# Performance work log

Hardware: AMD Instinct MI355X
Metric: run time of the kernel (lower is better)

## Reference

```python
import jax, jax.numpy as jnp
import numpy as np

D_MODEL = 1024
NUM_HEADS = 16
HEAD_DIM = D_MODEL // NUM_HEADS


def setup_inputs() -> dict:
    key = jax.random.key(0)
    ks = jax.random.split(key, 5)
    B, S = 4, 2048
    x = jax.random.normal(ks[0], (B, S, D_MODEL), dtype=jnp.float32)
    scale = 1.0 / np.sqrt(D_MODEL)
    qkv_w = jax.random.normal(ks[1], (3 * D_MODEL, D_MODEL), dtype=jnp.float32) * scale
    qkv_b = jnp.zeros((3 * D_MODEL,), dtype=jnp.float32)
    out_w = jax.random.normal(ks[2], (D_MODEL, D_MODEL), dtype=jnp.float32) * scale
    out_b = jnp.zeros((D_MODEL,), dtype=jnp.float32)
    return {"x": x, "qkv_w": qkv_w, "qkv_b": qkv_b, "out_w": out_w, "out_b": out_b}


def reference(x, qkv_w, qkv_b, out_w, out_b):
    B, S, _ = x.shape
    # qkv projection (torch Linear: x @ W.T + b)
    qkv = x @ qkv_w.T + qkv_b  # [B, S, 3*D]
    q, k, v = jnp.split(qkv, 3, axis=-1)
    # [B, H, S, hd]
    q = q.reshape(B, S, NUM_HEADS, HEAD_DIM).transpose(0, 2, 1, 3)
    k = k.reshape(B, S, NUM_HEADS, HEAD_DIM).transpose(0, 2, 1, 3)
    v = v.reshape(B, S, NUM_HEADS, HEAD_DIM).transpose(0, 2, 1, 3)
    scores = jnp.einsum('bhqd,bhkd->bhqk', q, k) / np.sqrt(HEAD_DIM).astype(np.float32)
    attn = jax.nn.softmax(scores, axis=-1)
    context = jnp.einsum('bhqk,bhkd->bhqd', attn, v)  # [B, H, S, hd]
    context = context.transpose(0, 2, 1, 3).reshape(B, S, D_MODEL)
    return context @ out_w.T + out_b
```

## Files before the change

### kernel.cpp

```cpp
#include <hip/hip_runtime.h>
#include <hip/hip_bf16.h>
#include <math.h>

#define D_MODEL 1024
#define NHEADS  16
#define HDIM    64
#define BATCH   4
#define SLEN    2048
#define MROWS   (BATCH * SLEN)
#define QKV_N   (3 * D_MODEL)

typedef __attribute__((ext_vector_type(8))) short bhalf8;
typedef __attribute__((ext_vector_type(4))) float f32x4;

#if __has_builtin(__builtin_amdgcn_exp2f)
#define EXP2(x) __builtin_amdgcn_exp2f(x)
#else
#define EXP2(x) exp2f(x)
#endif

#define MFMA16(a, b, c) __builtin_amdgcn_mfma_f32_16x16x32_bf16((a), (b), (c), 0, 0, 0)

static __device__ __forceinline__ unsigned short f2bf(float f) {
    unsigned int u = __builtin_bit_cast(unsigned int, f);
    unsigned int r = (u + 0x7FFFu + ((u >> 16) & 1u)) >> 16;
    return (unsigned short)r;
}

static __device__ __forceinline__ unsigned int pack_hi16(float lo, float hi) {
    return __builtin_amdgcn_perm(__builtin_bit_cast(unsigned int, hi),
                                 __builtin_bit_cast(unsigned int, lo),
                                 0x07060302u);
}

static __device__ __forceinline__ void load_lds16(const void* g, void* l) {
    __builtin_amdgcn_global_load_lds(
        (const __attribute__((address_space(1))) void*)g,
        (__attribute__((address_space(3))) void*)l, 16, 0, 0);
}

#define FENCE() __asm__ volatile("" ::: "memory")
#define BARRIER() do { FENCE();                                   \
        __builtin_amdgcn_sched_barrier(0);                        \
        __builtin_amdgcn_s_barrier();                             \
        __builtin_amdgcn_sched_barrier(0); FENCE(); } while (0)
#define WAIT_VM(N)   __asm__ volatile("s_waitcnt vmcnt(" #N ")" ::: "memory")
#define WAIT_LGKM0() __asm__ volatile("s_waitcnt lgkmcnt(0)" ::: "memory")

__global__ __launch_bounds__(256) void cast_f32_bf16(
    const float* __restrict__ in, unsigned short* __restrict__ out, int n)
{
    int i = (blockIdx.x * 256 + threadIdx.x) * 4;
    if (i < n) {
        float4 v = *(const float4*)(in + i);
        ushort4 o;
        o.x = f2bf(v.x); o.y = f2bf(v.y); o.z = f2bf(v.z); o.w = f2bf(v.w);
        *(ushort4*)(out + i) = o;
    }
}

template<bool BF16OUT>
__global__ __launch_bounds__(256) void gemm_mfma_bt(
    const unsigned short* __restrict__ A,
    const unsigned short* __restrict__ W,
    const float* __restrict__ bias,
    void* __restrict__ outv,
    int M, int N, int K, int qcols, float qscale)
{
    __shared__ __align__(16) unsigned short As[128 * 32];
    __shared__ __align__(16) unsigned short Bs[128 * 32];

    const int tid  = threadIdx.x;
    const int bm   = blockIdx.y * 128;
    const int bn   = blockIdx.x * 128;
    const int wave = tid >> 6;
    const int lane = tid & 63;
    const int m16  = lane & 15;
    const int quad = lane >> 4;
    const int wm   = (wave & 1) * 64;
    const int wn   = (wave >> 1) * 64;

    const int r0 = tid >> 2;
    const int s0 = tid & 3;
    const int g0 = (s0 - (r0 >> 1)) & 3;
    const int g1 = (s0 - ((r0 + 64) >> 1)) & 3;

    const size_t arow0 = (size_t)(bm + r0) * K + g0 * 8;
    const size_t arow1 = (size_t)(bm + r0 + 64) * K + g1 * 8;
    const size_t brow0 = (size_t)(bn + r0) * K + g0 * 8;
    const size_t brow1 = (size_t)(bn + r0 + 64) * K + g1 * 8;

    f32x4 acc[4][4];
    f32x4 zero = {0.f, 0.f, 0.f, 0.f};
#pragma unroll
    for (int i = 0; i < 4; ++i)
#pragma unroll
        for (int j = 0; j < 4; ++j) acc[i][j] = zero;

    for (int kt = 0; kt < K; kt += 32) {
        __syncthreads();
        load_lds16(A + arow0 + kt, As + tid * 8);
        load_lds16(A + arow1 + kt, As + 2048 + tid * 8);
        load_lds16(W + brow0 + kt, Bs + tid * 8);
        load_lds16(W + brow1 + kt, Bs + 2048 + tid * 8);
        __asm__ volatile("s_waitcnt vmcnt(0)" ::: "memory");
        __syncthreads();

        bhalf8 af[4], bf[4];
#pragma unroll
        for (int i = 0; i < 4; ++i) {
            int ra = wm + i * 16 + m16;
            int sa = (quad + (ra >> 1)) & 3;
            af[i] = *(const bhalf8*)&As[ra * 32 + sa * 8];
        }
#pragma unroll
        for (int j = 0; j < 4; ++j) {
            int rb = wn + j * 16 + m16;
            int sb = (quad + (rb >> 1)) & 3;
            bf[j] = *(const bhalf8*)&Bs[rb * 32 + sb * 8];
        }
#pragma unroll
        for (int i = 0; i < 4; ++i)
#pragma unroll
            for (int j = 0; j < 4; ++j)
                acc[i][j] = __builtin_amdgcn_mfma_f32_16x16x32_bf16(
                    af[i], bf[j], acc[i][j], 0, 0, 0);
    }

    float bj[4], scj[4];
#pragma unroll
    for (int j = 0; j < 4; ++j) {
        int col = bn + wn + j * 16 + m16;
        bj[j]  = bias[col];
        scj[j] = (col < qcols) ? qscale : 1.0f;
    }

#pragma unroll
    for (int i = 0; i < 4; ++i) {
#pragma unroll
        for (int r = 0; r < 4; ++r) {
            size_t row = (size_t)(bm + wm + i * 16 + quad * 4 + r);
            if (BF16OUT) {
                unsigned short* dst = (unsigned short*)outv + row * N + bn + wn;
#pragma unroll
                for (int j = 0; j < 4; ++j)
                    dst[j * 16 + m16] = f2bf((acc[i][j][r] + bj[j]) * scj[j]);
            } else {
                float* dst = (float*)outv + row * N + bn + wn;
#pragma unroll
                for (int j = 0; j < 4; ++j)
                    dst[j * 16 + m16] = (acc[i][j][r] + bj[j]) * scj[j];
            }
        }
    }
}

__global__ __launch_bounds__(256, 4) void attn_mfma_kernel(
    const unsigned short* __restrict__ qkv, unsigned short* __restrict__ ctx)
{
    const int orig = blockIdx.x + (blockIdx.y << 4) + (blockIdx.z << 8);
    const int flat = ((orig & 7) << 7) | (orig >> 3);
    const int qt = flat & 15;
    const int h  = (flat >> 4) & 15;
    const int b  = flat >> 8;

    const int tid  = threadIdx.x;
    const int wave = tid >> 6;
    const int lane = tid & 63;
    const int m16  = lane & 15;
    const int quad = lane >> 4;

    __shared__ __align__(16) unsigned short K_lds[64 * 64];
    __shared__ __align__(16) unsigned short Vt_lds[64 * 72];
    __shared__ __align__(16) unsigned short QP_lds[4 * 32 * 72];

    const int srow  = tid >> 3;
    const int sslot = tid & 7;
    const int gk    = (sslot - srow) & 7;

    const int u    = tid & 31;
    const int k0   = (u & 15) | ((u & 16) << 1);
    const int idx0 = (u & 15) * 4 + ((u >> 4) << 1);
    const int vd0  = (tid >> 5) * 8;

    const unsigned short* kPtr =
        qkv + ((size_t)b * SLEN) * QKV_N + D_MODEL + h * HDIM
            + (size_t)srow * QKV_N + gk * 8;
    const unsigned short* vPtr0 =
        qkv + ((size_t)b * SLEN) * QKV_N + 2 * D_MODEL + h * HDIM
            + (size_t)k0 * QKV_N + vd0;
    const unsigned short* vPtr1 = vPtr0 + (size_t)16 * QKV_N;

    uint4 va_A, vb_A, va_B, vb_B;

#define ISSUE_K(T) do {                                                      \
        const unsigned short* kb_ = kPtr + (size_t)(T) * 64 * QKV_N;         \
        load_lds16(kb_,                        K_lds + tid * 8);             \
        load_lds16(kb_ + (size_t)32 * QKV_N,   K_lds + 2048 + tid * 8);      \
    } while (0)

#define ISSUE_V(T, VA, VB) do {                                              \
        VA = *(const uint4*)(vPtr0 + (size_t)(T) * 64 * QKV_N);              \
        VB = *(const uint4*)(vPtr1 + (size_t)(T) * 64 * QKV_N);              \
    } while (0)

#define WRITE_V(VA, VB) do {                                                                         \
        *(unsigned int*)&Vt_lds[(vd0 + 0) * 72 + idx0] = __builtin_amdgcn_perm(VB.x, VA.x, 0x05040100u); \
        *(unsigned int*)&Vt_lds[(vd0 + 1) * 72 + idx0] = __builtin_amdgcn_perm(VB.x, VA.x, 0x07060302u); \
        *(unsigned int*)&Vt_lds[(vd0 + 2) * 72 + idx0] = __builtin_amdgcn_perm(VB.y, VA.y, 0x05040100u); \
        *(unsigned int*)&Vt_lds[(vd0 + 3) * 72 + idx0] = __builtin_amdgcn_perm(VB.y, VA.y, 0x07060302u); \
        *(unsigned int*)&Vt_lds[(vd0 + 4) * 72 + idx0] = __builtin_amdgcn_perm(VB.z, VA.z, 0x05040100u); \
        *(unsigned int*)&Vt_lds[(vd0 + 5) * 72 + idx0] = __builtin_amdgcn_perm(VB.z, VA.z, 0x07060302u); \
        *(unsigned int*)&Vt_lds[(vd0 + 6) * 72 + idx0] = __builtin_amdgcn_perm(VB.w, VA.w, 0x05040100u); \
        *(unsigned int*)&Vt_lds[(vd0 + 7) * 72 + idx0] = __builtin_amdgcn_perm(VB.w, VA.w, 0x07060302u); \
    } while (0)

    {
        const unsigned short* qbase =
            qkv + (size_t)(b * SLEN + qt * 128) * QKV_N + h * HDIM;
#pragma unroll
        for (int c = 0; c < 4; ++c) {
            int r = c * 32 + srow;
            int g = (sslot - r) & 7;
            load_lds16(qbase + (size_t)r * QKV_N + g * 8,
                       QP_lds + c * 2048 + tid * 8);
        }
    }
    ISSUE_K(0);
    ISSUE_V(0, va_A, vb_A);
    WAIT_VM(2);
    BARRIER();

    bhalf8 qf[2][2];
#pragma unroll
    for (int qi = 0; qi < 2; ++qi) {
        int rq = wave * 32 + qi * 16 + m16;
#pragma unroll
        for (int ks = 0; ks < 2; ++ks) {
            int slot = (ks * 4 + quad + rq) & 7;
            qf[qi][ks] = *(const bhalf8*)&QP_lds[rq * 64 + slot * 8];
        }
    }

    WAIT_VM(0);
    WRITE_V(va_A, vb_A);
    ISSUE_V(1, va_B, vb_B);
    WAIT_LGKM0();
    BARRIER();

    f32x4 zero = {0.f, 0.f, 0.f, 0.f};
    f32x4 oacc[2][4], oacc_l[2];
#pragma unroll
    for (int qi = 0; qi < 2; ++qi) {
        oacc_l[qi] = zero;
#pragma unroll
        for (int dt = 0; dt < 4; ++dt) oacc[qi][dt] = zero;
    }

    bhalf8 ones;
#pragma unroll
    for (int i = 0; i < 8; ++i) ones[i] = (short)0x3F80;

    unsigned short* P = &QP_lds[wave * (32 * 72)];
    f32x4 sacc[2][4];

#define QKT_PHASE() do {                                                     \
        _Pragma("unroll")                                                    \
        for (int qi = 0; qi < 2; ++qi)                                       \
            _Pragma("unroll")                                                \
            for (int nt = 0; nt < 4; ++nt) sacc[qi][nt] = zero;              \
        __builtin_amdgcn_s_setprio(1);                                       \
        _Pragma("unroll")                                                    \
        for (int ks = 0; ks < 2; ++ks) {                                     \
            _Pragma("unroll")                                                \
            for (int nt = 0; nt < 4; ++nt) {                                 \
                int rk = nt * 16 + m16;                                      \
                int slot = (ks * 4 + quad + rk) & 7;                         \
                bhalf8 kf = *(const bhalf8*)&K_lds[rk * 64 + slot * 8];      \
                sacc[0][nt] = MFMA16(qf[0][ks], kf, sacc[0][nt]);            \
                sacc[1][nt] = MFMA16(qf[1][ks], kf, sacc[1][nt]);            \
            }                                                                \
        }                                                                    \
        __builtin_amdgcn_s_setprio(0);                                       \
    } while (0)

#define SOFTMAX_PHASE() do {                                                 \
        _Pragma("unroll")                                                    \
        for (int qi = 0; qi < 2; ++qi) {                                     \
            _Pragma("unroll")                                                \
            for (int r = 0; r < 4; ++r) {                                    \
                float p0 = EXP2(sacc[qi][0][r]);                             \
                float p1 = EXP2(sacc[qi][1][r]);                             \
                float p2 = EXP2(sacc[qi][2][r]);                             \
                float p3 = EXP2(sacc[qi][3][r]);                             \
                uint2 w;                                                     \
                w.x = pack_hi16(p0, p1);                                     \
                w.y = pack_hi16(p2, p3);                                     \
                *(uint2*)&P[(qi * 16 + quad * 4 + r) * 72 + m16 * 4] = w;    \
            }                                                                \
        }                                                                    \
        WAIT_LGKM0();                                                        \
        __builtin_amdgcn_sched_barrier(0);                                   \
    } while (0)

#define PV_PHASE() do {                                                      \
        __builtin_amdgcn_s_setprio(1);                                       \
        _Pragma("unroll")                                                    \
        for (int ks = 0; ks < 2; ++ks) {                                     \
            bhalf8 pf0 = *(const bhalf8*)&P[(m16)      * 72 + ks * 32 + quad * 8]; \
            bhalf8 pf1 = *(const bhalf8*)&P[(16 + m16) * 72 + ks * 32 + quad * 8]; \
            oacc_l[0] = MFMA16(pf0, ones, oacc_l[0]);                        \
            oacc_l[1] = MFMA16(pf1, ones, oacc_l[1]);                        \
            _Pragma("unroll")                                                \
            for (int dt = 0; dt < 4; ++dt) {                                 \
                bhalf8 vf = *(const bhalf8*)&Vt_lds[(dt * 16 + m16) * 72 + ks * 32 + quad * 8]; \
                oacc[0][dt] = MFMA16(pf0, vf, oacc[0][dt]);                  \
                oacc[1][dt] = MFMA16(pf1, vf, oacc[1][dt]);                  \
            }                                                                \
        }                                                                    \
        __builtin_amdgcn_s_setprio(0);                                       \
    } while (0)

#define TILE_FULL(T, VAW, VBW, VAL, VBL) do {                                \
        QKT_PHASE();                                                         \
        BARRIER();                     \
        ISSUE_K((T) + 1);                                                    \
        SOFTMAX_PHASE();                                                     \
        PV_PHASE();                                                          \
        BARRIER();                     \
        WAIT_VM(2);                    \
        WRITE_V(VAW, VBW);                                                   \
        ISSUE_V((T) + 2, VAL, VBL);                                          \
        WAIT_VM(2);                    \
        WAIT_LGKM0();                                                        \
        BARRIER();                     \
    } while (0)

    for (int t2 = 0; t2 < 30; t2 += 2) {
        TILE_FULL(t2,     va_B, vb_B, va_A, vb_A);
        TILE_FULL(t2 + 1, va_A, vb_A, va_B, vb_B);
    }

    QKT_PHASE();
    BARRIER();
    ISSUE_K(31);
    SOFTMAX_PHASE();
    PV_PHASE();
    BARRIER();
    WAIT_VM(2);
    WRITE_V(va_B, vb_B);
    WAIT_VM(0);
    WAIT_LGKM0();
    BARRIER();

    QKT_PHASE();
    SOFTMAX_PHASE();
    PV_PHASE();

#undef TILE_FULL
#undef PV_PHASE
#undef SOFTMAX_PHASE
#undef QKT_PHASE
#undef WRITE_V
#undef ISSUE_V
#undef ISSUE_K

#pragma unroll
    for (int qi = 0; qi < 2; ++qi) {
#pragma unroll
        for (int r = 0; r < 4; ++r) {
            float inv = 1.0f / oacc_l[qi][r];
            int row = b * SLEN + qt * 128 + wave * 32 + qi * 16 + quad * 4 + r;
            unsigned short* dst = ctx + (size_t)row * D_MODEL + h * HDIM;
#pragma unroll
            for (int dt = 0; dt < 4; ++dt)
                dst[dt * 16 + m16] = f2bf(oacc[qi][dt][r] * inv);
        }
    }
}

extern "C" void kernel_launch(void* const* d_in, const int* in_sizes, int n_in,
                              void* d_out, int out_size, void* d_ws, size_t ws_size,
                              hipStream_t stream)
{
    const float* x     = (const float*)d_in[0];
    const float* qkv_w = (const float*)d_in[1];
    const float* qkv_b = (const float*)d_in[2];
    const float* out_w = (const float*)d_in[3];
    const float* out_b = (const float*)d_in[4];
    float* out = (float*)d_out;

    unsigned short* xbf  = (unsigned short*)d_ws;
    unsigned short* wqkv = xbf  + (size_t)MROWS * D_MODEL;
    unsigned short* wout = wqkv + (size_t)QKV_N * D_MODEL;
    unsigned short* qkv  = wout + (size_t)D_MODEL * D_MODEL;
    unsigned short* ctx  = qkv  + (size_t)MROWS * QKV_N;

    {
        int n;
        n = MROWS * D_MODEL;
        cast_f32_bf16<<<n / 1024, 256, 0, stream>>>(x, xbf, n);
        n = QKV_N * D_MODEL;
        cast_f32_bf16<<<n / 1024, 256, 0, stream>>>(qkv_w, wqkv, n);
        n = D_MODEL * D_MODEL;
        cast_f32_bf16<<<n / 1024, 256, 0, stream>>>(out_w, wout, n);
    }

    const float QSCALE = 0.125f * 1.44269504088896f;

    {
        dim3 grid(QKV_N / 128, MROWS / 128);
        gemm_mfma_bt<true><<<grid, 256, 0, stream>>>(xbf, wqkv, qkv_b, qkv,
                                                     MROWS, QKV_N, D_MODEL,
                                                     D_MODEL, QSCALE);
    }

    {
        dim3 grid(SLEN / 128, NHEADS, BATCH);
        attn_mfma_kernel<<<grid, 256, 0, stream>>>(qkv, ctx);
    }

    {
        dim3 grid(D_MODEL / 128, MROWS / 128);
        gemm_mfma_bt<false><<<grid, 256, 0, stream>>>(ctx, wout, out_b, out,
                                                      MROWS, D_MODEL, D_MODEL,
                                                      0, 1.0f);
    }
}
```

Baseline: 280.7 us.

## Double-buffer K/V tiles in attention and merge cast kernels into one launch

The attention kernel now keeps two LDS buffers for K and transposed V. This lets the next K tile be prefetched before the QK^T phase and removes two of the three barriers per tile, overlapping loads with compute. Separately, the three fp32-to-bf16 cast launches are merged into one kernel to cut launch overhead. The extra LDS (about 17 KB more per block) may lower occupancy below the declared 4 blocks per CU.

```diff
diff --git a/kernel.cpp b/kernel.cpp
--- a/kernel.cpp
+++ b/kernel.cpp
@@ -47,16 +47,25 @@
 #define WAIT_VM(N)   __asm__ volatile("s_waitcnt vmcnt(" #N ")" ::: "memory")
 #define WAIT_LGKM0() __asm__ volatile("s_waitcnt lgkmcnt(0)" ::: "memory")
 
-__global__ __launch_bounds__(256) void cast_f32_bf16(
-    const float* __restrict__ in, unsigned short* __restrict__ out, int n)
+__global__ __launch_bounds__(256) void cast3_f32_bf16(
+    const float* __restrict__ a, unsigned short* __restrict__ oa, int na,
+    const float* __restrict__ b, unsigned short* __restrict__ ob, int nb,
+    const float* __restrict__ c, unsigned short* __restrict__ oc, int nc)
 {
     int i = (blockIdx.x * 256 + threadIdx.x) * 4;
-    if (i < n) {
-        float4 v = *(const float4*)(in + i);
-        ushort4 o;
-        o.x = f2bf(v.x); o.y = f2bf(v.y); o.z = f2bf(v.z); o.w = f2bf(v.w);
-        *(ushort4*)(out + i) = o;
-    }
+    const float* src;
+    unsigned short* dst;
+    if (i < na)           { src = a + i;            dst = oa + i; }
+    else if (i < na + nb) { src = b + (i - na);     dst = ob + (i - na); }
+    else {
+        int j = i - na - nb;
+        if (j >= nc) return;
+        src = c + j; dst = oc + j;
+    }
+    float4 v = *(const float4*)src;
+    ushort4 o;
+    o.x = f2bf(v.x); o.y = f2bf(v.y); o.z = f2bf(v.z); o.w = f2bf(v.w);
+    *(ushort4*)dst = o;
 }
 
 template<bool BF16OUT>
@@ -170,8 +179,8 @@
     const int m16  = lane & 15;
     const int quad = lane >> 4;
 
-    __shared__ __align__(16) unsigned short K_lds[64 * 64];
-    __shared__ __align__(16) unsigned short Vt_lds[64 * 72];
+    __shared__ __align__(16) unsigned short K_lds[2][64 * 64];
+    __shared__ __align__(16) unsigned short Vt_lds[2][64 * 72];
     __shared__ __align__(16) unsigned short QP_lds[4 * 32 * 72];
 
     const int srow  = tid >> 3;
@@ -193,10 +202,10 @@
 
     uint4 va_A, vb_A, va_B, vb_B;
 
-#define ISSUE_K(T) do {                                                      \
+#define ISSUE_K(T, BUF) do {                                                 \
         const unsigned short* kb_ = kPtr + (size_t)(T) * 64 * QKV_N;         \
-        load_lds16(kb_,                        K_lds + tid * 8);             \
-        load_lds16(kb_ + (size_t)32 * QKV_N,   K_lds + 2048 + tid * 8);      \
+        load_lds16(kb_,                      &K_lds[BUF][tid * 8]);          \
+        load_lds16(kb_ + (size_t)32 * QKV_N, &K_lds[BUF][2048 + tid * 8]);   \
     } while (0)
 
 #define ISSUE_V(T, VA, VB) do {                                              \
@@ -204,15 +213,15 @@
         VB = *(const uint4*)(vPtr1 + (size_t)(T) * 64 * QKV_N);              \
     } while (0)
 
-#define WRITE_V(VA, VB) do {                                                                         \
-        *(unsigned int*)&Vt_lds[(vd0 + 0) * 72 + idx0] = __builtin_amdgcn_perm(VB.x, VA.x, 0x05040100u); \
-        *(unsigned int*)&Vt_lds[(vd0 + 1) * 72 + idx0] = __builtin_amdgcn_perm(VB.x, VA.x, 0x07060302u); \
-        *(unsigned int*)&Vt_lds[(vd0 + 2) * 72 + idx0] = __builtin_amdgcn_perm(VB.y, VA.y, 0x05040100u); \
-        *(unsigned int*)&Vt_lds[(vd0 + 3) * 72 + idx0] = __builtin_amdgcn_perm(VB.y, VA.y, 0x07060302u); \
-        *(unsigned int*)&Vt_lds[(vd0 + 4) * 72 + idx0] = __builtin_amdgcn_perm(VB.z, VA.z, 0x05040100u); \
-        *(unsigned int*)&Vt_lds[(vd0 + 5) * 72 + idx0] = __builtin_amdgcn_perm(VB.z, VA.z, 0x07060302u); \
-        *(unsigned int*)&Vt_lds[(vd0 + 6) * 72 + idx0] = __builtin_amdgcn_perm(VB.w, VA.w, 0x05040100u); \
-        *(unsigned int*)&Vt_lds[(vd0 + 7) * 72 + idx0] = __builtin_amdgcn_perm(VB.w, VA.w, 0x07060302u); \
+#define WRITE_V(BUF, VA, VB) do {                                                                        \
+        *(unsigned int*)&Vt_lds[BUF][(vd0 + 0) * 72 + idx0] = __builtin_amdgcn_perm(VB.x, VA.x, 0x05040100u); \
+        *(unsigned int*)&Vt_lds[BUF][(vd0 + 1) * 72 + idx0] = __builtin_amdgcn_perm(VB.x, VA.x, 0x07060302u); \
+        *(unsigned int*)&Vt_lds[BUF][(vd0 + 2) * 72 + idx0] = __builtin_amdgcn_perm(VB.y, VA.y, 0x05040100u); \
+        *(unsigned int*)&Vt_lds[BUF][(vd0 + 3) * 72 + idx0] = __builtin_amdgcn_perm(VB.y, VA.y, 0x07060302u); \
+        *(unsigned int*)&Vt_lds[BUF][(vd0 + 4) * 72 + idx0] = __builtin_amdgcn_perm(VB.z, VA.z, 0x05040100u); \
+        *(unsigned int*)&Vt_lds[BUF][(vd0 + 5) * 72 + idx0] = __builtin_amdgcn_perm(VB.z, VA.z, 0x07060302u); \
+        *(unsigned int*)&Vt_lds[BUF][(vd0 + 6) * 72 + idx0] = __builtin_amdgcn_perm(VB.w, VA.w, 0x05040100u); \
+        *(unsigned int*)&Vt_lds[BUF][(vd0 + 7) * 72 + idx0] = __builtin_amdgcn_perm(VB.w, VA.w, 0x07060302u); \
     } while (0)
 
     {
@@ -226,7 +235,7 @@
                        QP_lds + c * 2048 + tid * 8);
         }
     }
-    ISSUE_K(0);
+    ISSUE_K(0, 0);
     ISSUE_V(0, va_A, vb_A);
     WAIT_VM(2);
     BARRIER();
@@ -243,7 +252,7 @@
     }
 
     WAIT_VM(0);
-    WRITE_V(va_A, vb_A);
+    WRITE_V(0, va_A, vb_A);
     ISSUE_V(1, va_B, vb_B);
     WAIT_LGKM0();
     BARRIER();
@@ -264,7 +273,7 @@
     unsigned short* P = &QP_lds[wave * (32 * 72)];
     f32x4 sacc[2][4];
 
-#define QKT_PHASE() do {                                                     \
+#define QKT_PHASE(CUR) do {                                                  \
         _Pragma("unroll")                                                    \
         for (int qi = 0; qi < 2; ++qi)                                       \
             _Pragma("unroll")                                                \
@@ -276,7 +285,7 @@
             for (int nt = 0; nt < 4; ++nt) {                                 \
                 int rk = nt * 16 + m16;                                      \
                 int slot = (ks * 4 + quad + rk) & 7;                         \
-                bhalf8 kf = *(const bhalf8*)&K_lds[rk * 64 + slot * 8];      \
+                bhalf8 kf = *(const bhalf8*)&K_lds[CUR][rk * 64 + slot * 8]; \
                 sacc[0][nt] = MFMA16(qf[0][ks], kf, sacc[0][nt]);            \
                 sacc[1][nt] = MFMA16(qf[1][ks], kf, sacc[1][nt]);            \
             }                                                                \
@@ -303,7 +312,7 @@
         __builtin_amdgcn_sched_barrier(0);                                   \
     } while (0)
 
-#define PV_PHASE() do {                                                      \
+#define PV_PHASE(CUR) do {                                                   \
         __builtin_amdgcn_s_setprio(1);                                       \
         _Pragma("unroll")                                                    \
         for (int ks = 0; ks < 2; ++ks) {                                     \
@@ -313,7 +322,7 @@
             oacc_l[1] = MFMA16(pf1, ones, oacc_l[1]);                        \
             _Pragma("unroll")                                                \
             for (int dt = 0; dt < 4; ++dt) {                                 \
-                bhalf8 vf = *(const bhalf8*)&Vt_lds[(dt * 16 + m16) * 72 + ks * 32 + quad * 8]; \
+                bhalf8 vf = *(const bhalf8*)&Vt_lds[CUR][(dt * 16 + m16) * 72 + ks * 32 + quad * 8]; \
                 oacc[0][dt] = MFMA16(pf0, vf, oacc[0][dt]);                  \
                 oacc[1][dt] = MFMA16(pf1, vf, oacc[1][dt]);                  \
             }                                                                \
@@ -321,43 +330,39 @@
         __builtin_amdgcn_s_setprio(0);                                       \
     } while (0)
 
-#define TILE_FULL(T, VAW, VBW, VAL, VBL) do {                                \
-        QKT_PHASE();                                                         \
-        BARRIER();                     \
-        ISSUE_K((T) + 1);                                                    \
+#define TILE(T, CUR, NXT, VWA, VWB, VLA, VLB) do {                           \
+        ISSUE_K((T) + 1, NXT);               \
+        QKT_PHASE(CUR);                                                      \
         SOFTMAX_PHASE();                                                     \
-        PV_PHASE();                                                          \
-        BARRIER();                     \
-        WAIT_VM(2);                    \
-        WRITE_V(VAW, VBW);                                                   \
-        ISSUE_V((T) + 2, VAL, VBL);                                          \
-        WAIT_VM(2);                    \
+        PV_PHASE(CUR);                                                       \
+        WAIT_VM(2);                      \
+        WRITE_V(NXT, VWA, VWB);             \
+        ISSUE_V((T) + 2, VLA, VLB);                                          \
+        WAIT_VM(2);                     \
         WAIT_LGKM0();                                                        \
-        BARRIER();                     \
+        BARRIER();                               \
     } while (0)
 
     for (int t2 = 0; t2 < 30; t2 += 2) {
-        TILE_FULL(t2,     va_B, vb_B, va_A, vb_A);
-        TILE_FULL(t2 + 1, va_A, vb_A, va_B, vb_B);
-    }
-
-    QKT_PHASE();
-    BARRIER();
-    ISSUE_K(31);
+        TILE(t2,     0, 1, va_B, vb_B, va_A, vb_A);
+        TILE(t2 + 1, 1, 0, va_A, vb_A, va_B, vb_B);
+    }
+
+    ISSUE_K(31, 1);
+    QKT_PHASE(0);
     SOFTMAX_PHASE();
-    PV_PHASE();
-    BARRIER();
+    PV_PHASE(0);
     WAIT_VM(2);
-    WRITE_V(va_B, vb_B);
+    WRITE_V(1, va_B, vb_B);
     WAIT_VM(0);
     WAIT_LGKM0();
     BARRIER();
 
-    QKT_PHASE();
+    QKT_PHASE(1);
     SOFTMAX_PHASE();
-    PV_PHASE();
-
-#undef TILE_FULL
+    PV_PHASE(1);
+
+#undef TILE
 #undef PV_PHASE
 #undef SOFTMAX_PHASE
 #undef QKT_PHASE
@@ -397,13 +402,12 @@
     unsigned short* ctx  = qkv  + (size_t)MROWS * QKV_N;
 
     {
-        int n;
-        n = MROWS * D_MODEL;
-        cast_f32_bf16<<<n / 1024, 256, 0, stream>>>(x, xbf, n);
-        n = QKV_N * D_MODEL;
-        cast_f32_bf16<<<n / 1024, 256, 0, stream>>>(qkv_w, wqkv, n);
-        n = D_MODEL * D_MODEL;
-        cast_f32_bf16<<<n / 1024, 256, 0, stream>>>(out_w, wout, n);
+        const int na = MROWS * D_MODEL;
+        const int nb = QKV_N * D_MODEL;
+        const int nc = D_MODEL * D_MODEL;
+        const int total = na + nb + nc;
+        cast3_f32_bf16<<<total / 1024, 256, 0, stream>>>(
+            x, xbf, na, qkv_w, wqkv, nb, out_w, wout, nc);
     }
 
     const float QSCALE = 0.125f * 1.44269504088896f;
```

After: 298.3 us. +6.3%, slower.

## Use 8 waves per attention block and fuse the three cast kernels

Applied to the files above, without the earlier changes.

The attention kernel now launches 512 threads, and each of its 8 waves handles 16 query rows instead of 32. Q fragments are read straight from global memory into registers instead of being staged through LDS, and the per-thread K and V load widths are halved to match the larger thread count. The three fp32-to-bf16 cast launches are merged into one kernel that picks its source by index range. The goal is more waves to hide latency and fewer launches, at the cost of less K/V reuse per wave and more barrier traffic per tile.

```diff
diff --git a/kernel.cpp b/kernel.cpp
--- a/kernel.cpp
+++ b/kernel.cpp
@@ -47,16 +47,25 @@
 #define WAIT_VM(N)   __asm__ volatile("s_waitcnt vmcnt(" #N ")" ::: "memory")
 #define WAIT_LGKM0() __asm__ volatile("s_waitcnt lgkmcnt(0)" ::: "memory")
 
-__global__ __launch_bounds__(256) void cast_f32_bf16(
-    const float* __restrict__ in, unsigned short* __restrict__ out, int n)
+__global__ __launch_bounds__(256) void cast3_f32_bf16(
+    const float* __restrict__ a, unsigned short* __restrict__ oa, int na,
+    const float* __restrict__ b, unsigned short* __restrict__ ob, int nb,
+    const float* __restrict__ c, unsigned short* __restrict__ oc, int nc)
 {
     int i = (blockIdx.x * 256 + threadIdx.x) * 4;
-    if (i < n) {
-        float4 v = *(const float4*)(in + i);
-        ushort4 o;
-        o.x = f2bf(v.x); o.y = f2bf(v.y); o.z = f2bf(v.z); o.w = f2bf(v.w);
-        *(ushort4*)(out + i) = o;
-    }
+    const float* src;
+    unsigned short* dst;
+    if (i < na)           { src = a + i;            dst = oa + i; }
+    else if (i < na + nb) { src = b + (i - na);     dst = ob + (i - na); }
+    else {
+        int j = i - na - nb;
+        if (j >= nc) return;
+        src = c + j; dst = oc + j;
+    }
+    float4 v = *(const float4*)src;
+    ushort4 o;
+    o.x = f2bf(v.x); o.y = f2bf(v.y); o.z = f2bf(v.z); o.w = f2bf(v.w);
+    *(ushort4*)dst = o;
 }
 
 template<bool BF16OUT>
@@ -155,7 +164,7 @@
     }
 }
 
-__global__ __launch_bounds__(256, 4) void attn_mfma_kernel(
+__global__ __launch_bounds__(512, 8) void attn_mfma_kernel(
     const unsigned short* __restrict__ qkv, unsigned short* __restrict__ ctx)
 {
     const int orig = blockIdx.x + (blockIdx.y << 4) + (blockIdx.z << 8);
@@ -172,7 +181,7 @@
 
     __shared__ __align__(16) unsigned short K_lds[64 * 64];
     __shared__ __align__(16) unsigned short Vt_lds[64 * 72];
-    __shared__ __align__(16) unsigned short QP_lds[4 * 32 * 72];
+    __shared__ __align__(16) unsigned short P_lds[8 * 16 * 72];
 
     const int srow  = tid >> 3;
     const int sslot = tid & 7;
@@ -181,7 +190,7 @@
     const int u    = tid & 31;
     const int k0   = (u & 15) | ((u & 16) << 1);
     const int idx0 = (u & 15) * 4 + ((u >> 4) << 1);
-    const int vd0  = (tid >> 5) * 8;
+    const int vd0  = (tid >> 5) * 4;
 
     const unsigned short* kPtr =
         qkv + ((size_t)b * SLEN) * QKV_N + D_MODEL + h * HDIM
@@ -191,57 +200,33 @@
             + (size_t)k0 * QKV_N + vd0;
     const unsigned short* vPtr1 = vPtr0 + (size_t)16 * QKV_N;
 
-    uint4 va_A, vb_A, va_B, vb_B;
+    uint2 va_A, vb_A, va_B, vb_B;
 
 #define ISSUE_K(T) do {                                                      \
-        const unsigned short* kb_ = kPtr + (size_t)(T) * 64 * QKV_N;         \
-        load_lds16(kb_,                        K_lds + tid * 8);             \
-        load_lds16(kb_ + (size_t)32 * QKV_N,   K_lds + 2048 + tid * 8);      \
+        load_lds16(kPtr + (size_t)(T) * 64 * QKV_N, K_lds + tid * 8);        \
     } while (0)
 
 #define ISSUE_V(T, VA, VB) do {                                              \
-        VA = *(const uint4*)(vPtr0 + (size_t)(T) * 64 * QKV_N);              \
-        VB = *(const uint4*)(vPtr1 + (size_t)(T) * 64 * QKV_N);              \
-    } while (0)
-
-#define WRITE_V(VA, VB) do {                                                                         \
+        VA = *(const uint2*)(vPtr0 + (size_t)(T) * 64 * QKV_N);              \
+        VB = *(const uint2*)(vPtr1 + (size_t)(T) * 64 * QKV_N);              \
+    } while (0)
+
+#define WRITE_V(VA, VB) do {                                                                          \
         *(unsigned int*)&Vt_lds[(vd0 + 0) * 72 + idx0] = __builtin_amdgcn_perm(VB.x, VA.x, 0x05040100u); \
         *(unsigned int*)&Vt_lds[(vd0 + 1) * 72 + idx0] = __builtin_amdgcn_perm(VB.x, VA.x, 0x07060302u); \
         *(unsigned int*)&Vt_lds[(vd0 + 2) * 72 + idx0] = __builtin_amdgcn_perm(VB.y, VA.y, 0x05040100u); \
         *(unsigned int*)&Vt_lds[(vd0 + 3) * 72 + idx0] = __builtin_amdgcn_perm(VB.y, VA.y, 0x07060302u); \
-        *(unsigned int*)&Vt_lds[(vd0 + 4) * 72 + idx0] = __builtin_amdgcn_perm(VB.z, VA.z, 0x05040100u); \
-        *(unsigned int*)&Vt_lds[(vd0 + 5) * 72 + idx0] = __builtin_amdgcn_perm(VB.z, VA.z, 0x07060302u); \
-        *(unsigned int*)&Vt_lds[(vd0 + 6) * 72 + idx0] = __builtin_amdgcn_perm(VB.w, VA.w, 0x05040100u); \
-        *(unsigned int*)&Vt_lds[(vd0 + 7) * 72 + idx0] = __builtin_amdgcn_perm(VB.w, VA.w, 0x07060302u); \
-    } while (0)
-
+    } while (0)
+
+    bhalf8 qf[2];
     {
         const unsigned short* qbase =
-            qkv + (size_t)(b * SLEN + qt * 128) * QKV_N + h * HDIM;
-#pragma unroll
-        for (int c = 0; c < 4; ++c) {
-            int r = c * 32 + srow;
-            int g = (sslot - r) & 7;
-            load_lds16(qbase + (size_t)r * QKV_N + g * 8,
-                       QP_lds + c * 2048 + tid * 8);
-        }
+            qkv + (size_t)(b * SLEN + qt * 128 + wave * 16 + m16) * QKV_N + h * HDIM;
+        qf[0] = *(const bhalf8*)(qbase + quad * 8);
+        qf[1] = *(const bhalf8*)(qbase + 32 + quad * 8);
     }
     ISSUE_K(0);
     ISSUE_V(0, va_A, vb_A);
-    WAIT_VM(2);
-    BARRIER();
-
-    bhalf8 qf[2][2];
-#pragma unroll
-    for (int qi = 0; qi < 2; ++qi) {
-        int rq = wave * 32 + qi * 16 + m16;
-#pragma unroll
-        for (int ks = 0; ks < 2; ++ks) {
-            int slot = (ks * 4 + quad + rq) & 7;
-            qf[qi][ks] = *(const bhalf8*)&QP_lds[rq * 64 + slot * 8];
-        }
-    }
-
     WAIT_VM(0);
     WRITE_V(va_A, vb_A);
     ISSUE_V(1, va_B, vb_B);
@@ -249,26 +234,21 @@
     BARRIER();
 
     f32x4 zero = {0.f, 0.f, 0.f, 0.f};
-    f32x4 oacc[2][4], oacc_l[2];
-#pragma unroll
-    for (int qi = 0; qi < 2; ++qi) {
-        oacc_l[qi] = zero;
-#pragma unroll
-        for (int dt = 0; dt < 4; ++dt) oacc[qi][dt] = zero;
-    }
+    f32x4 oacc[4], oacc_l;
+    oacc_l = zero;
+#pragma unroll
+    for (int dt = 0; dt < 4; ++dt) oacc[dt] = zero;
 
     bhalf8 ones;
 #pragma unroll
     for (int i = 0; i < 8; ++i) ones[i] = (short)0x3F80;
 
-    unsigned short* P = &QP_lds[wave * (32 * 72)];
-    f32x4 sacc[2][4];
+    unsigned short* P = &P_lds[wave * (16 * 72)];
+    f32x4 sacc[4];
 
 #define QKT_PHASE() do {                                                     \
         _Pragma("unroll")                                                    \
-        for (int qi = 0; qi < 2; ++qi)                                       \
-            _Pragma("unroll")                                                \
-            for (int nt = 0; nt < 4; ++nt) sacc[qi][nt] = zero;              \
+        for (int nt = 0; nt < 4; ++nt) sacc[nt] = zero;                      \
         __builtin_amdgcn_s_setprio(1);                                       \
         _Pragma("unroll")                                                    \
         for (int ks = 0; ks < 2; ++ks) {                                     \
@@ -277,8 +257,7 @@
                 int rk = nt * 16 + m16;                                      \
                 int slot = (ks * 4 + quad + rk) & 7;                         \
                 bhalf8 kf = *(const bhalf8*)&K_lds[rk * 64 + slot * 8];      \
-                sacc[0][nt] = MFMA16(qf[0][ks], kf, sacc[0][nt]);            \
-                sacc[1][nt] = MFMA16(qf[1][ks], kf, sacc[1][nt]);            \
+                sacc[nt] = MFMA16(qf[ks], kf, sacc[nt]);                     \
             }                                                                \
         }                                                                    \
         __builtin_amdgcn_s_setprio(0);                                       \
@@ -286,18 +265,15 @@
 
 #define SOFTMAX_PHASE() do {                                                 \
         _Pragma("unroll")                                                    \
-        for (int qi = 0; qi < 2; ++qi) {                                     \
-            _Pragma("unroll")                                                \
-            for (int r = 0; r < 4; ++r) {                                    \
-                float p0 = EXP2(sacc[qi][0][r]);                             \
-                float p1 = EXP2(sacc[qi][1][r]);                             \
-                float p2 = EXP2(sacc[qi][2][r]);                             \
-                float p3 = EXP2(sacc[qi][3][r]);                             \
-                uint2 w;                                                     \
-                w.x = pack_hi16(p0, p1);                                     \
-                w.y = pack_hi16(p2, p3);                                     \
-                *(uint2*)&P[(qi * 16 + quad * 4 + r) * 72 + m16 * 4] = w;    \
-            }                                                                \
+        for (int r = 0; r < 4; ++r) {                                        \
+            float p0 = EXP2(sacc[0][r]);                                     \
+            float p1 = EXP2(sacc[1][r]);                                     \
+            float p2 = EXP2(sacc[2][r]);                                     \
+            float p3 = EXP2(sacc[3][r]);                                     \
+            uint2 w;                                                         \
+            w.x = pack_hi16(p0, p1);                                         \
+            w.y = pack_hi16(p2, p3);                                         \
+            *(uint2*)&P[(quad * 4 + r) * 72 + m16 * 4] = w;                  \
         }                                                                    \
         WAIT_LGKM0();                                                        \
         __builtin_amdgcn_sched_barrier(0);                                   \
@@ -307,33 +283,30 @@
         __builtin_amdgcn_s_setprio(1);                                       \
         _Pragma("unroll")                                                    \
         for (int ks = 0; ks < 2; ++ks) {                                     \
-            bhalf8 pf0 = *(const bhalf8*)&P[(m16)      * 72 + ks * 32 + quad * 8]; \
-            bhalf8 pf1 = *(const bhalf8*)&P[(16 + m16) * 72 + ks * 32 + quad * 8]; \
-            oacc_l[0] = MFMA16(pf0, ones, oacc_l[0]);                        \
-            oacc_l[1] = MFMA16(pf1, ones, oacc_l[1]);                        \
+            bhalf8 pf = *(const bhalf8*)&P[m16 * 72 + ks * 32 + quad * 8];   \
+            oacc_l = MFMA16(pf, ones, oacc_l);                               \
             _Pragma("unroll")                                                \
             for (int dt = 0; dt < 4; ++dt) {                                 \
                 bhalf8 vf = *(const bhalf8*)&Vt_lds[(dt * 16 + m16) * 72 + ks * 32 + quad * 8]; \
-                oacc[0][dt] = MFMA16(pf0, vf, oacc[0][dt]);                  \
-                oacc[1][dt] = MFMA16(pf1, vf, oacc[1][dt]);                  \
+                oacc[dt] = MFMA16(pf, vf, oacc[dt]);                         \
             }                                                                \
         }                                                                    \
         __builtin_amdgcn_s_setprio(0);                                       \
     } while (0)
 
-#define TILE_FULL(T, VAW, VBW, VAL, VBL) do {                                \
+#define TILE_FULL(T, VWA, VWB, VLA, VLB) do {                                \
         QKT_PHASE();                                                         \
         BARRIER();                     \
         ISSUE_K((T) + 1);                                                    \
         SOFTMAX_PHASE();                                                     \
         PV_PHASE();                                                          \
         BARRIER();                     \
-        WAIT_VM(2);                    \
-        WRITE_V(VAW, VBW);                                                   \
-        ISSUE_V((T) + 2, VAL, VBL);                                          \
-        WAIT_VM(2);                    \
+        WAIT_VM(1);                     \
+        WRITE_V(VWA, VWB);                                                   \
+        ISSUE_V((T) + 2, VLA, VLB);                                          \
+        WAIT_VM(2);                     \
         WAIT_LGKM0();                                                        \
-        BARRIER();                     \
+        BARRIER();                           \
     } while (0)
 
     for (int t2 = 0; t2 < 30; t2 += 2) {
@@ -347,7 +320,7 @@
     SOFTMAX_PHASE();
     PV_PHASE();
     BARRIER();
-    WAIT_VM(2);
+    WAIT_VM(1);
     WRITE_V(va_B, vb_B);
     WAIT_VM(0);
     WAIT_LGKM0();
@@ -366,16 +339,13 @@
 #undef ISSUE_K
 
 #pragma unroll
-    for (int qi = 0; qi < 2; ++qi) {
-#pragma unroll
-        for (int r = 0; r < 4; ++r) {
-            float inv = 1.0f / oacc_l[qi][r];
-            int row = b * SLEN + qt * 128 + wave * 32 + qi * 16 + quad * 4 + r;
-            unsigned short* dst = ctx + (size_t)row * D_MODEL + h * HDIM;
-#pragma unroll
-            for (int dt = 0; dt < 4; ++dt)
-                dst[dt * 16 + m16] = f2bf(oacc[qi][dt][r] * inv);
-        }
+    for (int r = 0; r < 4; ++r) {
+        float inv = 1.0f / oacc_l[r];
+        int row = b * SLEN + qt * 128 + wave * 16 + quad * 4 + r;
+        unsigned short* dst = ctx + (size_t)row * D_MODEL + h * HDIM;
+#pragma unroll
+        for (int dt = 0; dt < 4; ++dt)
+            dst[dt * 16 + m16] = f2bf(oacc[dt][r] * inv);
     }
 }
 
@@ -397,13 +367,12 @@
     unsigned short* ctx  = qkv  + (size_t)MROWS * QKV_N;
 
     {
-        int n;
-        n = MROWS * D_MODEL;
-        cast_f32_bf16<<<n / 1024, 256, 0, stream>>>(x, xbf, n);
-        n = QKV_N * D_MODEL;
-        cast_f32_bf16<<<n / 1024, 256, 0, stream>>>(qkv_w, wqkv, n);
-        n = D_MODEL * D_MODEL;
-        cast_f32_bf16<<<n / 1024, 256, 0, stream>>>(out_w, wout, n);
+        const int na = MROWS * D_MODEL;
+        const int nb = QKV_N * D_MODEL;
+        const int nc = D_MODEL * D_MODEL;
+        const int total = na + nb + nc;
+        cast3_f32_bf16<<<total / 1024, 256, 0, stream>>>(
+            x, xbf, na, qkv_w, wqkv, nb, out_w, wout, nc);
     }
 
     const float QSCALE = 0.125f * 1.44269504088896f;
@@ -417,7 +386,7 @@
 
     {
         dim3 grid(SLEN / 128, NHEADS, BATCH);
-        attn_mfma_kernel<<<grid, 256, 0, stream>>>(qkv, ctx);
+        attn_mfma_kernel<<<grid, 512, 0, stream>>>(qkv, ctx);
     }
 
     {
```

Measured after the change: 373.4 us. 33.0% more time.
